# Kernel tuning notes

Hardware: AMD Instinct MI355X
Metric: run time of the kernel (lower is better)

Reference implementation:

```python
import jax, jax.numpy as jnp
import numpy as np

K = 10          # number of neighbors (init kwarg k)
NUM_CLASSES = 100  # label vocabulary (targets drawn in [0, 100))


def setup_inputs() -> dict:
    key = jax.random.key(0)
    k1, k2, k3 = jax.random.split(key, 3)
    X = jax.random.normal(k1, (1024, 512), dtype=jnp.float32)
    data = jax.random.normal(k2, (50000, 512), dtype=jnp.float32)
    targets = jax.random.randint(k3, (50000,), 0, NUM_CLASSES, dtype=jnp.int64)
    return {"X": X, "data": data, "targets": targets}


def reference(X, data, targets):
    # Pairwise L2 distance (p=2 path of the module), computed via the
    x2 = jnp.sum(X * X, axis=1, keepdims=True)              # [Q, 1]
    d2 = jnp.sum(data * data, axis=1)                        # [N]
    sq = x2 + d2[None, :] - 2.0 * (X @ data.T)               # [Q, N]
    dist = jnp.sqrt(jnp.maximum(sq, 0.0))                    # torch.norm(p1-p2, p=2)

    # torch: sort distances ascending, take first k indices -> top-k smallest.
    _, idx = jax.lax.top_k(-dist, K)                         # [Q, K]
    labels = targets[idx]                                    # [Q, K]

    # torch.mode over the k neighbor labels: histogram + argmax.
    # argmax picks the first (smallest) class on ties, matching torch.mode.
    counts = jax.nn.one_hot(labels, NUM_CLASSES, dtype=jnp.float32).sum(axis=1)  # [Q, C]
    pred = jnp.argmax(counts, axis=1).astype(jnp.float32)    # [Q]
    return pred
```

## Files before the change

kernel.cpp:

```cpp
#include <hip/hip_runtime.h>
#include <math.h>
#include <limits.h>

#define QN 1024
#define NN 50000
#define NPAD 50048
#define DD 512
#define KNN 10
#define NT 128
#define QTB 128
#define BK 32
#define NS 391
#define QB 8
#define NSAMP 63
#define NREST (NS - NSAMP)
#define CAP 512
#define SLACK 4.0f
#define LCAP 1152

#define WS_D2  0
#define WS_TAU 50048
#define WS_CNT (WS_TAU + 1024)
#define WS_XH  (WS_CNT + 1024)
#define WS_CKS (WS_XH + QN * DD / 2)
#define WS_BUF (WS_CKS + QN * NSAMP * KNN * 2)
#define WS_DH  (WS_BUF + QN * CAP * 2)
#define WS_END (WS_DH + NS * 16 * 2048)

typedef __attribute__((ext_vector_type(8))) short short8;
typedef __attribute__((ext_vector_type(4))) float f32x4;
typedef unsigned long long u64;

__device__ __forceinline__ u64 mkkey(float f, int idx) {
  unsigned u = __float_as_uint(f);
  unsigned m = u ^ ((unsigned)((int)u >> 31) | 0x80000000u);
  return ((u64)m << 32) | (unsigned)idx;
}

__device__ __forceinline__ float keyhi_f(unsigned m) {
  unsigned u = (m & 0x80000000u) ? (m ^ 0x80000000u) : ~m;
  return __uint_as_float(u);
}

__device__ __forceinline__ unsigned cvth(float x, float y) {
  unsigned ux = __float_as_uint(x), uy = __float_as_uint(y);
  unsigned rx = ux + 0x7fffu + ((ux >> 16) & 1u);
  unsigned ry = uy + 0x7fffu + ((uy >> 16) & 1u);
  return (rx >> 16) | (ry & 0xffff0000u);
}

__device__ __forceinline__ void glds16(const void* g, void* l) {
  __builtin_amdgcn_global_load_lds(
      (const __attribute__((address_space(1))) unsigned*)g,
      (__attribute__((address_space(3))) unsigned*)l, 16, 0, 0);
}

__device__ __forceinline__ void ins10(u64* kl, u64 k) {
#pragma unroll
  for (int u = 0; u < KNN; u++) {
    u64 lo = (k < kl[u]) ? k : kl[u];
    u64 hi = (k < kl[u]) ? kl[u] : k;
    kl[u] = lo; k = hi;
  }
}

__global__ __launch_bounds__(256) void conv_kernel(
    const float* __restrict__ dat, const float* __restrict__ Xm,
    float* __restrict__ ws) {
  if ((int)blockIdx.x >= NS) {
    const int g = ((int)blockIdx.x - NS) * 256 + threadIdx.x;
    const int b = g >> 10, kc = (g >> 6) & 15, l = g & 63;
    const int row = b * 16 + (l & 15);
    const int col = kc * 32 + (l >> 4) * 8;
    const float4* p = (const float4*)(Xm + (size_t)row * DD + col);
    float4 v0 = p[0], v1 = p[1];
    ((uint4*)(ws + WS_XH))[g] = make_uint4(
        cvth(v0.x, v0.y), cvth(v0.z, v0.w), cvth(v1.x, v1.y), cvth(v1.z, v1.w));
    return;
  }
  const int slice = blockIdx.x;
  const int t = threadIdx.x;
  const int row = t >> 1, h2 = t & 1;
  const int gr = slice * NT + row;
  const int r15 = row & 15;
  float s = 0.f;
#pragma unroll
  for (int kc8 = 0; kc8 < 8; kc8++) {
    const int kc = h2 * 8 + kc8;
    float4 v[8];
    if (gr < NN) {
      const float4* src = (const float4*)(dat + (size_t)gr * DD + kc * 32);
#pragma unroll
      for (int j = 0; j < 8; j++) v[j] = src[j];
    } else {
#pragma unroll
      for (int j = 0; j < 8; j++) v[j] = make_float4(0.f, 0.f, 0.f, 0.f);
    }
    unsigned hw[16];
#pragma unroll
    for (int j = 0; j < 8; j++) {
      s = fmaf(v[j].x, v[j].x, s); s = fmaf(v[j].y, v[j].y, s);
      s = fmaf(v[j].z, v[j].z, s); s = fmaf(v[j].w, v[j].w, s);
      hw[2 * j]     = cvth(v[j].x, v[j].y);
      hw[2 * j + 1] = cvth(v[j].z, v[j].w);
    }
    uint4* dhp = (uint4*)((unsigned char*)(ws + WS_DH) +
                          (((size_t)slice * 16 + kc) * 8 + (row >> 4)) * 1024);
#pragma unroll
    for (int qd = 0; qd < 4; qd++)
      dhp[qd * 16 + r15] = make_uint4(hw[4 * qd], hw[4 * qd + 1], hw[4 * qd + 2], hw[4 * qd + 3]);
  }
  s += __shfl_xor(s, 1, 64);
  if (h2 == 0) ws[WS_D2 + gr] = (gr < NN) ? s : __builtin_inff();
}

struct StageT { unsigned char bh[8192]; };
struct EpiT  { float sq[64][132]; };
struct ListT { u64 kl[64][4][KNN]; };

template <int MODE> struct SmemSel {
  union U { StageT s; EpiT e; ListT l; };
};
template <> struct SmemSel<1> {
  struct U { StageT s; float tau[128]; };
};

template <int PRE, int MODE>
__global__ __launch_bounds__(256, 3) void knn_chunk(
    const float* __restrict__ dat, float* __restrict__ ws, int soff) {
  __shared__ __align__(16) typename SmemSel<MODE>::U sm;
  int bqx, bsy;
  if (MODE == 1 && (gridDim.y & 7) == 0) {
    const int n = (int)(blockIdx.y * gridDim.x + blockIdx.x);
    const int m = n >> 3;
    const int ypx = (int)(gridDim.y >> 3);
    bqx = m & 7;
    bsy = (n & 7) * ypx + (m >> 3);
  } else {
    bqx = blockIdx.x; bsy = blockIdx.y;
  }
  const int qbase = bqx * QTB;
  const int slice = bsy + soff;
  const int nbase = slice * NT;
  const int t = threadIdx.x;
  const int lane = t & 63, wave = t >> 6;
  const int wn = wave & 1, wq = wave >> 1;
  const unsigned char* dh = (const unsigned char*)(ws + WS_DH);
  const char* xfh = (const char*)(ws + WS_XH);
  const int abase = (((bqx * 8 + wq * 4) * 16) * 64 + lane) * 16;

  f32x4 acc[4][4];
#pragma unroll
  for (int i = 0; i < 4; i++)
#pragma unroll
    for (int j = 0; j < 4; j++) acc[i][j] = (f32x4)0.f;

  auto stageB = [&](int kc) {
#pragma unroll
    for (int i = 0; i < 2; i++) {
      int p = wave * 2 + i;
      const unsigned char* g = dh +
          (((size_t)slice * 16 + kc) * 8 + p) * 1024 + lane * 16;
      glds16(g, sm.s.bh + p * 1024);
    }
  };

  if (PRE) {
    stageB(0);
    for (int kc = 0; kc < 16; kc++) {
      short8 fah[4];
#pragma unroll
      for (int i = 0; i < 4; i++)
        fah[i] = *(const short8*)(xfh + abase + i * 16384 + kc * 1024);
      __syncthreads();
      const int fragoff = lane * 16;
      short8 fbh[4];
#pragma unroll
      for (int i = 0; i < 4; i++)
        fbh[i] = *(const short8*)(sm.s.bh + (wn * 4 + i) * 1024 + fragoff);
      __syncthreads();
      if (kc < 15) stageB(kc + 1);
#pragma unroll
      for (int mt = 0; mt < 4; mt++)
#pragma unroll
        for (int nt = 0; nt < 4; nt++)
          acc[mt][nt] = __builtin_amdgcn_mfma_f32_16x16x32_bf16(fah[mt], fbh[nt], acc[mt][nt], 0, 0, 0);
    }
  } else {
    const int brow = t >> 1, bh_half = t & 1;
    const int bgr = nbase + brow;
    const int bpanel = (brow >> 4) * 1024;
    const int bchunk = (brow & 15) * 16;
    for (int kc = 0; kc < 16; kc++) {
      const int kk = kc * BK;
      short8 fah[4];
#pragma unroll
      for (int i = 0; i < 4; i++)
        fah[i] = *(const short8*)(xfh + abase + i * 16384 + kc * 1024);
      __syncthreads();
      {
        float4 v0 = make_float4(0.f, 0.f, 0.f, 0.f), v1 = v0, v2 = v0, v3 = v0;
        if (bgr < NN) {
          const float4* src = (const float4*)(dat + (size_t)bgr * DD + kk + bh_half * 16);
          v0 = src[0]; v1 = src[1]; v2 = src[2]; v3 = src[3];
        }
        unsigned char* bhp = sm.s.bh + bpanel;
        *(uint4*)(bhp + (2 * bh_half) * 256 + bchunk) =
            make_uint4(cvth(v0.x, v0.y), cvth(v0.z, v0.w), cvth(v1.x, v1.y), cvth(v1.z, v1.w));
        *(uint4*)(bhp + (2 * bh_half + 1) * 256 + bchunk) =
            make_uint4(cvth(v2.x, v2.y), cvth(v2.z, v2.w), cvth(v3.x, v3.y), cvth(v3.z, v3.w));
      }
      __syncthreads();
      const int fragoff = lane * 16;
      short8 fbh[4];
#pragma unroll
      for (int i = 0; i < 4; i++)
        fbh[i] = *(const short8*)(sm.s.bh + (wn * 4 + i) * 1024 + fragoff);
      __syncthreads();
#pragma unroll
      for (int mt = 0; mt < 4; mt++)
#pragma unroll
        for (int nt = 0; nt < 4; nt++)
          acc[mt][nt] = __builtin_amdgcn_mfma_f32_16x16x32_bf16(fah[mt], fbh[nt], acc[mt][nt], 0, 0, 0);
    }
  }

  if constexpr (MODE == 0) {
#pragma unroll
    for (int pass = 0; pass < 2; pass++) {
      __syncthreads();
      if (wq == pass) {
#pragma unroll
        for (int nt = 0; nt < 4; nt++) {
          int col = wn * 64 + nt * 16 + (lane & 15);
          float d2v = ws[WS_D2 + nbase + col];
#pragma unroll
          for (int mt = 0; mt < 4; mt++)
#pragma unroll
            for (int rg = 0; rg < 4; rg++) {
              int lr = mt * 16 + (lane >> 4) * 4 + rg;
              sm.e.sq[lr][col] = fmaf(-2.f, acc[mt][nt][rg], d2v);
            }
        }
      }
      __syncthreads();
      {
        const int r = t >> 2, s = t & 3;
        u64 kl[KNN];
#pragma unroll
        for (int u = 0; u < KNN; u++) kl[u] = ~0ull;
        for (int jj = 0; jj < 32; jj++) {
          int c = s * 32 + ((jj + r + 8 * s) & 31);
          float v = sm.e.sq[r][c];
          ins10(kl, mkkey(v, nbase + c));
        }
        __syncthreads();
#pragma unroll
        for (int u = 0; u < KNN; u++) sm.l.kl[r][s][u] = kl[u];
      }
      __syncthreads();
      if (t < 64) {
        u64* dst = ((u64*)(ws + WS_CKS)) +
                   ((size_t)(qbase + pass * 64 + t) * NSAMP + blockIdx.y) * KNN;
        int h0 = 0, h1 = 0, h2 = 0, h3 = 0;
        for (int pick = 0; pick < KNN; pick++) {
          u64 k0 = sm.l.kl[t][0][h0], k1 = sm.l.kl[t][1][h1];
          u64 k2 = sm.l.kl[t][2][h2], k3 = sm.l.kl[t][3][h3];
          u64 best = k0; int bm = 0;
          if (k1 < best) { best = k1; bm = 1; }
          if (k2 < best) { best = k2; bm = 2; }
          if (k3 < best) { best = k3; bm = 3; }
          dst[pick] = best;
          h0 += (bm == 0); h1 += (bm == 1); h2 += (bm == 2); h3 += (bm == 3);
        }
      }
    }
  } else {
    if (t < 128) sm.tau[t] = ws[WS_TAU + qbase + t];
    __syncthreads();
    unsigned* cnt = (unsigned*)(ws + WS_CNT);
    u64* buf = (u64*)(ws + WS_BUF);
    float d2v[4];
#pragma unroll
    for (int nt = 0; nt < 4; nt++)
      d2v[nt] = ws[WS_D2 + nbase + wn * 64 + nt * 16 + (lane & 15)];
#pragma unroll
    for (int mt = 0; mt < 4; mt++)
#pragma unroll
      for (int rg = 0; rg < 4; rg++) {
        int row = wq * 64 + mt * 16 + (lane >> 4) * 4 + rg;
        float tr = sm.tau[row];
#pragma unroll
        for (int nt = 0; nt < 4; nt++) {
          float d = fmaf(-2.f, acc[mt][nt][rg], d2v[nt]);
          if (d < tr) {
            int col = nbase + wn * 64 + nt * 16 + (lane & 15);
            int q = qbase + row;
            unsigned slot = atomicAdd(cnt + q, 1u);
            if (slot < CAP) buf[(size_t)q * CAP + slot] = mkkey(d, col);
          }
        }
      }
  }
}

__global__ __launch_bounds__(64) void tau_kernel(float* __restrict__ ws) {
  const int q = blockIdx.x;
  const int t = threadIdx.x;
  const u64* samp = ((const u64*)(ws + WS_CKS)) + (size_t)q * NSAMP * KNN;
  const int NC = NSAMP * KNN;
  u64 kl[KNN];
#pragma unroll
  for (int u = 0; u < KNN; u++) kl[u] = ~0ull;
  for (int j = t; j < NC; j += 64) ins10(kl, samp[j]);
  __shared__ u64 wk[64][KNN];
  __shared__ u64 m2[8][KNN];
#pragma unroll
  for (int u = 0; u < KNN; u++) wk[t][u] = kl[u];
  __syncthreads();
  if (t < 8) {
    int h[8] = {0, 0, 0, 0, 0, 0, 0, 0};
    for (int pick = 0; pick < KNN; pick++) {
      u64 best = ~0ull; int bm = 0;
#pragma unroll
      for (int m = 0; m < 8; m++) {
        u64 km = wk[t * 8 + m][h[m]];
        if (km < best) { best = km; bm = m; }
      }
      m2[t][pick] = best;
#pragma unroll
      for (int m = 0; m < 8; m++) h[m] += (bm == m);
    }
  }
  __syncthreads();
  if (t == 0) {
    int h[8] = {0, 0, 0, 0, 0, 0, 0, 0};
    u64 best = 0;
    for (int pick = 0; pick < KNN; pick++) {
      best = ~0ull; int bm = 0;
#pragma unroll
      for (int m = 0; m < 8; m++) {
        u64 km = m2[m][h[m]];
        if (km < best) { best = km; bm = m; }
      }
#pragma unroll
      for (int m = 0; m < 8; m++) h[m] += (bm == m);
    }
    ws[WS_TAU + q] = keyhi_f((unsigned)(best >> 32)) + SLACK;
    ((unsigned*)(ws + WS_CNT))[q] = 0u;
  }
}

__global__ __launch_bounds__(256) void knn_final(
    const int* __restrict__ targets, const float* __restrict__ Xm,
    const float* __restrict__ dat, float* __restrict__ ws,
    float* __restrict__ out) {
  const int q = blockIdx.x;
  const int t = threadIdx.x;
  const int lane = t & 63, wave = t >> 6;
  __shared__ float qrow[DD];
  __shared__ unsigned lst[LCAP];
  __shared__ int nlist;
  __shared__ u64 wk4[4][KNN];
  if (t == 0) nlist = 0;
  if (t < 128) ((float4*)qrow)[t] = ((const float4*)(Xm + (size_t)q * DD))[t];
  __syncthreads();
  const float tr = ws[WS_TAU + q];
  const u64* samp = ((const u64*)(ws + WS_CKS)) + (size_t)q * NSAMP * KNN;
  for (int j = t; j < NSAMP * KNN; j += 256) {
    u64 k = samp[j];
    if (keyhi_f((unsigned)(k >> 32)) < tr) {
      int s_ = atomicAdd(&nlist, 1);
      if (s_ < LCAP) lst[s_] = (unsigned)k;
    }
  }
  unsigned c = ((const unsigned*)(ws + WS_CNT))[q];
  if (c > CAP) c = CAP;
  const u64* buf = ((const u64*)(ws + WS_BUF)) + (size_t)q * CAP;
  for (int j = t; j < (int)c; j += 256) {
    int s_ = atomicAdd(&nlist, 1);
    if (s_ < LCAP) lst[s_] = (unsigned)buf[j];
  }
  __syncthreads();
  const int n = nlist < LCAP ? nlist : LCAP;

  u64 kl[KNN];
#pragma unroll
  for (int u = 0; u < KNN; u++) kl[u] = ~0ull;
  const float4* qv = (const float4*)qrow;
  const float4 q0 = qv[lane * 2], q1 = qv[lane * 2 + 1];
  for (int j = wave; j < n; j += 4) {
    const unsigned idx = lst[j];
    const float4* xr = (const float4*)(dat + (size_t)idx * DD) + lane * 2;
    const float4 a0 = xr[0], a1 = xr[1];
    float p = a0.x * q0.x;
    p = fmaf(a0.y, q0.y, p); p = fmaf(a0.z, q0.z, p); p = fmaf(a0.w, q0.w, p);
    p = fmaf(a1.x, q1.x, p); p = fmaf(a1.y, q1.y, p);
    p = fmaf(a1.z, q1.z, p); p = fmaf(a1.w, q1.w, p);
#pragma unroll
    for (int s_ = 1; s_ < 64; s_ <<= 1) p += __shfl_xor(p, s_, 64);
    float d = fmaf(-2.f, p, ws[WS_D2 + idx]);
    ins10(kl, mkkey(d, (int)idx));
  }
  if (lane == 0)
#pragma unroll
    for (int u = 0; u < KNN; u++) wk4[wave][u] = kl[u];
  __syncthreads();
  if (t == 0) {
    int h[4] = {0, 0, 0, 0};
    int fi[KNN];
    for (int pick = 0; pick < KNN; pick++) {
      u64 best = ~0ull; int bm = 0;
#pragma unroll
      for (int m = 0; m < 4; m++) {
        u64 km = wk4[m][h[m]];
        if (km < best) { best = km; bm = m; }
      }
      fi[pick] = (int)(unsigned)(best & 0xffffffffu);
      h[bm]++;
    }
    int lab[KNN];
#pragma unroll
    for (int u = 0; u < KNN; u++) lab[u] = targets[fi[u]];
    int bc = 0, bl = INT_MAX;
#pragma unroll
    for (int i = 0; i < KNN; i++) {
      int cc = 0;
#pragma unroll
      for (int j = 0; j < KNN; j++) cc += (lab[j] == lab[i]) ? 1 : 0;
      if (cc > bc || (cc == bc && lab[i] < bl)) { bc = cc; bl = lab[i]; }
    }
    out[q] = (float)bl;
  }
}

extern "C" void kernel_launch(void* const* d_in, const int* in_sizes, int n_in,
                              void* d_out, int out_size, void* d_ws, size_t ws_size,
                              hipStream_t stream) {
  const float* Xm  = (const float*)d_in[0];
  const float* dat = (const float*)d_in[1];
  const int* targets = (const int*)d_in[2];
  float* out = (float*)d_out;
  float* ws  = (float*)d_ws;
  const bool pre = ws_size >= (size_t)WS_END * 4;

  hipLaunchKernelGGL(conv_kernel, dim3(NS + QN * DD / 8 / 256), dim3(256), 0,
                     stream, dat, Xm, ws);
  if (pre) {
    hipLaunchKernelGGL((knn_chunk<1, 0>), dim3(QB, NSAMP), dim3(256), 0, stream, dat, ws, 0);
    hipLaunchKernelGGL(tau_kernel, dim3(QN), dim3(64), 0, stream, ws);
    hipLaunchKernelGGL((knn_chunk<1, 1>), dim3(QB, NREST), dim3(256), 0, stream, dat, ws, NSAMP);
  } else {
    hipLaunchKernelGGL((knn_chunk<0, 0>), dim3(QB, NSAMP), dim3(256), 0, stream, dat, ws, 0);
    hipLaunchKernelGGL(tau_kernel, dim3(QN), dim3(64), 0, stream, ws);
    hipLaunchKernelGGL((knn_chunk<0, 1>), dim3(QB, NREST), dim3(256), 0, stream, dat, ws, NSAMP);
  }
  hipLaunchKernelGGL(knn_final, dim3(QN), dim3(256), 0, stream, targets, Xm, dat, ws, out);
}
```

Measured before the change: 317.5 us.

## Double-buffer B staging and prefetch A fragments in precomputed GEMM loop

```diff
diff --git a/kernel.cpp b/kernel.cpp
--- a/kernel.cpp
+++ b/kernel.cpp
@@ -12,7 +12,7 @@
 #define BK 32
 #define NS 391
 #define QB 8
-#define NSAMP 63
+#define NSAMP 31
 #define NREST (NS - NSAMP)
 #define CAP 512
 #define SLACK 4.0f
@@ -114,7 +114,7 @@
   if (h2 == 0) ws[WS_D2 + gr] = (gr < NN) ? s : __builtin_inff();
 }
 
-struct StageT { unsigned char bh[8192]; };
+struct StageT { unsigned char bh[2][8192]; };
 struct EpiT  { float sq[64][132]; };
 struct ListT { u64 kl[64][4][KNN]; };
 
@@ -155,37 +155,52 @@
 #pragma unroll
     for (int j = 0; j < 4; j++) acc[i][j] = (f32x4)0.f;
 
-  auto stageB = [&](int kc) {
+  auto stageB = [&](int kc, int bsel) {
 #pragma unroll
     for (int i = 0; i < 2; i++) {
       int p = wave * 2 + i;
       const unsigned char* g = dh +
           (((size_t)slice * 16 + kc) * 8 + p) * 1024 + lane * 16;
-      glds16(g, sm.s.bh + p * 1024);
+      glds16(g, sm.s.bh[bsel] + p * 1024);
     }
   };
 
   if (PRE) {
-    stageB(0);
+    short8 fah[4];
+    stageB(0, 0);
+#pragma unroll
+    for (int i = 0; i < 4; i++)
+      fah[i] = *(const short8*)(xfh + abase + i * 16384);
+#pragma unroll
     for (int kc = 0; kc < 16; kc++) {
-      short8 fah[4];
-#pragma unroll
-      for (int i = 0; i < 4; i++)
-        fah[i] = *(const short8*)(xfh + abase + i * 16384 + kc * 1024);
-      __syncthreads();
+      asm volatile("s_waitcnt vmcnt(0)" ::: "memory");
+      __builtin_amdgcn_s_barrier();
+      __builtin_amdgcn_sched_barrier(0);
+      asm volatile("" ::: "memory");
+      short8 fan[4];
+      if (kc < 15) {
+        stageB(kc + 1, (kc + 1) & 1);
+#pragma unroll
+        for (int i = 0; i < 4; i++)
+          fan[i] = *(const short8*)(xfh + abase + i * 16384 + (kc + 1) * 1024);
+      }
       const int fragoff = lane * 16;
       short8 fbh[4];
+      const unsigned char* bbase = sm.s.bh[kc & 1];
 #pragma unroll
       for (int i = 0; i < 4; i++)
-        fbh[i] = *(const short8*)(sm.s.bh + (wn * 4 + i) * 1024 + fragoff);
-      __syncthreads();
-      if (kc < 15) stageB(kc + 1);
+        fbh[i] = *(const short8*)(bbase + (wn * 4 + i) * 1024 + fragoff);
 #pragma unroll
       for (int mt = 0; mt < 4; mt++)
 #pragma unroll
         for (int nt = 0; nt < 4; nt++)
           acc[mt][nt] = __builtin_amdgcn_mfma_f32_16x16x32_bf16(fah[mt], fbh[nt], acc[mt][nt], 0, 0, 0);
-    }
+      if (kc < 15) {
+#pragma unroll
+        for (int i = 0; i < 4; i++) fah[i] = fan[i];
+      }
+    }
+    __syncthreads();
   } else {
     const int brow = t >> 1, bh_half = t & 1;
     const int bgr = nbase + brow;
@@ -204,7 +219,7 @@
           const float4* src = (const float4*)(dat + (size_t)bgr * DD + kk + bh_half * 16);
           v0 = src[0]; v1 = src[1]; v2 = src[2]; v3 = src[3];
         }
-        unsigned char* bhp = sm.s.bh + bpanel;
+        unsigned char* bhp = sm.s.bh[0] + bpanel;
         *(uint4*)(bhp + (2 * bh_half) * 256 + bchunk) =
             make_uint4(cvth(v0.x, v0.y), cvth(v0.z, v0.w), cvth(v1.x, v1.y), cvth(v1.z, v1.w));
         *(uint4*)(bhp + (2 * bh_half + 1) * 256 + bchunk) =
@@ -215,7 +230,7 @@
       short8 fbh[4];
 #pragma unroll
       for (int i = 0; i < 4; i++)
-        fbh[i] = *(const short8*)(sm.s.bh + (wn * 4 + i) * 1024 + fragoff);
+        fbh[i] = *(const short8*)(sm.s.bh[0] + (wn * 4 + i) * 1024 + fragoff);
       __syncthreads();
 #pragma unroll
       for (int mt = 0; mt < 4; mt++)
```

Result: slower. 358.1 us (+12.8%).
